# Performance work log

Hardware: AMD Instinct MI355X
Metric: run time of the kernel (lower is better)

The kernel has to match this reference:

```python
import jax, jax.numpy as jnp
import numpy as np

F_LEN = 21          # function_length
D_LEN = 41          # distribution_length
SLOPE = 1.0         # function_slope (nonzero -> tanh branch)
EPS = 1e-12         # torch F.normalize eps


def setup_inputs() -> dict:
    key = jax.random.key(0)
    k1, k2, k3, k4, k5 = jax.random.split(key, 5)
    B, L = 64, 2048
    S = F_LEN + D_LEN - 1  # 61, segment length required by the sliding slices
    lines_feature = jax.random.normal(k1, (B, L, 16), dtype=jnp.float32)
    pf = jax.random.uniform(k2, (B, L, S), dtype=jnp.float32, minval=0.1, maxval=1.0)
    pb = jax.random.uniform(k3, (B, L, S), dtype=jnp.float32, minval=0.1, maxval=1.0)
    slop = jax.random.uniform(k4, (B, L), dtype=jnp.float32, minval=0.5, maxval=2.5)
    amp = jax.random.uniform(k5, (B, L), dtype=jnp.float32, minval=0.1, maxval=0.4)
    return {
        "lines_feature": lines_feature,
        "lines_image_pf_segments": pf,
        "lines_image_pb_segments": pb,
        "lines_slop": slop,
        "lines_amplitude": amp,
    }


def reference(lines_feature, lines_image_pf_segments, lines_image_pb_segments,
              lines_slop, lines_amplitude):
    # lookup functions f/b over the function window  [B, L, F]
    x = jnp.arange(F_LEN, dtype=jnp.float32) - (F_LEN - 1) / 2.0
    lf = 0.5 - lines_amplitude[..., None] * jnp.tanh(x / (2.0 * lines_slop[..., None]))
    lb = 1.0 - lf

    # minimum variance floor (Laplace vs Gaussian)
    min_var_laplace = 1.0 / (2.0 * jnp.square(jnp.arctanh(2.0 * lines_amplitude)))
    min_var = jnp.maximum(min_var_laplace, lines_slop)

    # all D_LEN overlapping windows of length F_LEN, gathered in one shot
    idx = jnp.arange(D_LEN)[:, None] + jnp.arange(F_LEN)[None, :]   # [D, F]
    pf_win = lines_image_pf_segments[..., idx]                      # [B, L, D, F]
    pb_win = lines_image_pb_segments[..., idx]                      # [B, L, D, F]

    # log-domain product reduction over the window
    logp = jnp.log(pf_win * lf[..., None, :] + pb_win * lb[..., None, :]).sum(-1)
    dist = jnp.exp(logp)                                            # [B, L, D]

    # L1 normalize (torch.nn.functional.normalize, p=1)
    dist = dist / jnp.maximum(jnp.sum(jnp.abs(dist), axis=-1, keepdims=True), EPS)

    # line_distribution_extractor is identity pass-through of the distributions

    # Gaussian moment fit
    step = jnp.arange(D_LEN, dtype=jnp.float32)                     # [D]
    mean_tmp = jnp.sum(step * dist, axis=-1)                        # [B, L]
    var_tmp = jnp.sum(jnp.square(step - mean_tmp[..., None]) * dist, axis=-1)
    mean = mean_tmp - (D_LEN - 1) / 2.0
    var = jnp.maximum(var_tmp, min_var)
    return dist, mean, 1.0 / var
```

## Files before the change

### kernel.cpp

```cpp
#include <hip/hip_runtime.h>
#include <math.h>

#define F_LEN 21
#define D_LEN 41
#define S_LEN 61
#define ROWS 8
#define THREADS 64
#define NELEM (ROWS * S_LEN)
#define NV4   (NELEM / 4)
#define DOUT  (ROWS * D_LEN)
#define DV4   (DOUT / 4)

template <int CTRL>
__device__ __forceinline__ float dpp_add(float x) {
    int y = __builtin_amdgcn_update_dpp(0, __float_as_int(x), CTRL, 0xf, 0xf, true);
    return x + __int_as_float(y);
}
#define DPP_XOR1 0xB1
#define DPP_XOR2 0x4E
#define DPP_XOR7 0x141

__global__ __launch_bounds__(THREADS, 4) void bp_kernel(
    const float* __restrict__ pf_g, const float* __restrict__ pb_g,
    const float* __restrict__ slop_g, const float* __restrict__ amp_g,
    float* __restrict__ out_dist, float* __restrict__ out_mean,
    float* __restrict__ out_ivar)
{
    __shared__ float2 lds_fb[NELEM];

    const int tid  = threadIdx.x;
    const int rl   = tid >> 3;
    const int q    = tid & 7;
    const int row0 = blockIdx.x * ROWS;
    const int r    = row0 + rl;

    const float4* pf4 = (const float4*)(pf_g + (size_t)row0 * S_LEN);
    const float4* pb4 = (const float4*)(pb_g + (size_t)row0 * S_LEN);
    #pragma unroll
    for (int it = 0; it < 2; ++it) {
        int idx4 = it * THREADS + tid;
        if (idx4 < NV4) {
            float4 f = pf4[idx4];
            float4 b = pb4[idx4];
            lds_fb[idx4 * 4 + 0] = make_float2(f.x, b.x);
            lds_fb[idx4 * 4 + 1] = make_float2(f.y, b.y);
            lds_fb[idx4 * 4 + 2] = make_float2(f.z, b.z);
            lds_fb[idx4 * 4 + 3] = make_float2(f.w, b.w);
        }
    }

    const float a  = amp_g[r];
    const float sl = slop_g[r];

    float lf[F_LEN];
    lf[10] = 0.5f;
    {
        const float E1 = __expf(1.0f / sl);
        const float E2 = E1 * E1;
        const float E4 = E2 * E2;
        const float E8 = E4 * E4;
        float Ek[11];
        Ek[1] = E1;        Ek[2] = E2;        Ek[3] = E2 * E1;
        Ek[4] = E4;        Ek[5] = E4 * E1;   Ek[6] = E4 * E2;
        Ek[7] = E4 * Ek[3];Ek[8] = E8;        Ek[9] = E8 * E1;
        Ek[10] = E8 * E2;
        #pragma unroll
        for (int k = 1; k <= 10; ++k) {
            float rcp = __frcp_rn(Ek[k] + 1.0f);
            float dl  = a * ((Ek[k] - 1.0f) * rcp);
            lf[10 + k] = 0.5f - dl;
            lf[10 - k] = 0.5f + dl;
        }
    }

    __syncthreads();

    const int  d0   = q * 5;
    const bool has6 = (q == 7);
    const int  base = rl * S_LEN + d0;

    float prod[6] = {1.0f, 1.0f, 1.0f, 1.0f, 1.0f, 1.0f};
    #pragma unroll
    for (int i = 0; i < 26; ++i) {
        float2 fb = lds_fb[base + i];
        float  df = fb.x - fb.y;
        #pragma unroll
        for (int dp = 0; dp < 6; ++dp) {
            const int j = i - dp;
            if (j >= 0 && j < F_LEN) {
                float t = fmaf(lf[j], df, fb.y);
                if (dp == 5) t = has6 ? t : 1.0f;
                prod[dp] *= t;
            }
        }
    }

    const float df0 = (float)d0;
    float s0 = 0.0f, s1 = 0.0f, s2 = 0.0f;
    #pragma unroll
    for (int dp = 0; dp < 6; ++dp) {
        float p = prod[dp];
        if (dp == 5) p = has6 ? p : 0.0f;
        float dv = df0 + (float)dp;
        s0 += p;
        s1 += dv * p;
        s2 += dv * dv * p;
    }
    s0 = dpp_add<DPP_XOR1>(s0); s0 = dpp_add<DPP_XOR2>(s0); s0 = dpp_add<DPP_XOR7>(s0);
    s1 = dpp_add<DPP_XOR1>(s1); s1 = dpp_add<DPP_XOR2>(s1); s1 = dpp_add<DPP_XOR7>(s1);
    s2 = dpp_add<DPP_XOR1>(s2); s2 = dpp_add<DPP_XOR2>(s2); s2 = dpp_add<DPP_XOR7>(s2);

    const float inv      = 1.0f / fmaxf(s0, 1e-12f);
    const float mean_tmp = s1 * inv;
    const float m2       = s2 * inv;
    const float var_tmp  = fmaf(-mean_tmp, mean_tmp, m2);

    if (q == 0) {
        const float two_a = 2.0f * a;
        const float at    = 0.5f * __logf((1.0f + two_a) / (1.0f - two_a));
        const float min_v = fmaxf(0.5f / (at * at), sl);
        const float var   = fmaxf(var_tmp, min_v);
        out_mean[r] = mean_tmp - (float)((D_LEN - 1) / 2);
        out_ivar[r] = 1.0f / var;
    }

    __syncthreads();
    float* ldsd = (float*)lds_fb;
    #pragma unroll
    for (int dp = 0; dp < 5; ++dp)
        ldsd[rl * D_LEN + d0 + dp] = prod[dp] * inv;
    if (has6)
        ldsd[rl * D_LEN + 40] = prod[5] * inv;
    __syncthreads();

    const float4* ld4 = (const float4*)ldsd;
    float4* o4 = (float4*)(out_dist + (size_t)row0 * D_LEN);
    #pragma unroll
    for (int it = 0; it < 2; ++it) {
        int idx4 = it * THREADS + tid;
        if (idx4 < DV4) o4[idx4] = ld4[idx4];
    }
}

extern "C" void kernel_launch(void* const* d_in, const int* in_sizes, int n_in,
                              void* d_out, int out_size, void* d_ws, size_t ws_size,
                              hipStream_t stream) {
    const float* pf   = (const float*)d_in[1];
    const float* pb   = (const float*)d_in[2];
    const float* slop = (const float*)d_in[3];
    const float* amp  = (const float*)d_in[4];

    const int rows = in_sizes[3];

    float* out_dist = (float*)d_out;
    float* out_mean = out_dist + (size_t)rows * D_LEN;
    float* out_ivar = out_mean + rows;

    const int blocks = rows / ROWS;
    bp_kernel<<<blocks, THREADS, 0, stream>>>(pf, pb, slop, amp,
                                              out_dist, out_mean, out_ivar);
}
```

Before: 26.90 us.

## Process four tiles per block with double-buffered direct global-to-LDS loads

```diff
diff --git a/kernel.cpp b/kernel.cpp
--- a/kernel.cpp
+++ b/kernel.cpp
@@ -5,11 +5,12 @@
 #define D_LEN 41
 #define S_LEN 61
 #define ROWS 8
+#define TILES 4
 #define THREADS 64
-#define NELEM (ROWS * S_LEN)
-#define NV4   (NELEM / 4)
-#define DOUT  (ROWS * D_LEN)
-#define DV4   (DOUT / 4)
+#define TFLO (ROWS * S_LEN)
+#define TPAD 512
+#define DOUTT (ROWS * D_LEN)
+#define DV4T (DOUTT / 4)
 
 template <int CTRL>
 __device__ __forceinline__ float dpp_add(float x) {
@@ -20,125 +21,158 @@
 #define DPP_XOR2 0x4E
 #define DPP_XOR7 0x141
 
+__device__ __forceinline__ void gll16(const float* g, float* l) {
+    __builtin_amdgcn_global_load_lds(
+        (const __attribute__((address_space(1))) void*)g,
+        (__attribute__((address_space(3))) void*)l, 16, 0, 0);
+}
+
+__device__ __forceinline__ void stage_tile(const float* pf_g, const float* pb_g,
+                                           float* bufF, float* bufB,
+                                           int row0, int lane) {
+    const float* gf = pf_g + (size_t)row0 * S_LEN;
+    const float* gb = pb_g + (size_t)row0 * S_LEN;
+    gll16(gf + lane * 4, bufF);
+    gll16(gb + lane * 4, bufB);
+    if (lane < 58) {
+        gll16(gf + 256 + lane * 4, bufF + 256);
+        gll16(gb + 256 + lane * 4, bufB + 256);
+    }
+}
+
+#define FENCE() do { asm volatile("" ::: "memory"); \
+                     __builtin_amdgcn_sched_barrier(0); } while (0)
+
 __global__ __launch_bounds__(THREADS, 4) void bp_kernel(
     const float* __restrict__ pf_g, const float* __restrict__ pb_g,
     const float* __restrict__ slop_g, const float* __restrict__ amp_g,
     float* __restrict__ out_dist, float* __restrict__ out_mean,
     float* __restrict__ out_ivar)
 {
-    __shared__ float2 lds_fb[NELEM];
+    __shared__ float ldsF[2][TPAD];
+    __shared__ float ldsB[2][TPAD];
+    __shared__ float distL[DOUTT];
 
-    const int tid  = threadIdx.x;
-    const int rl   = tid >> 3;
-    const int q    = tid & 7;
-    const int row0 = blockIdx.x * ROWS;
-    const int r    = row0 + rl;
+    const int lane = threadIdx.x;
+    const int rl   = lane >> 3;
+    const int q    = lane & 7;
+    const int brow = blockIdx.x * (TILES * ROWS);
 
-    const float4* pf4 = (const float4*)(pf_g + (size_t)row0 * S_LEN);
-    const float4* pb4 = (const float4*)(pb_g + (size_t)row0 * S_LEN);
+    float aT[TILES], sT[TILES];
     #pragma unroll
-    for (int it = 0; it < 2; ++it) {
-        int idx4 = it * THREADS + tid;
-        if (idx4 < NV4) {
-            float4 f = pf4[idx4];
-            float4 b = pb4[idx4];
-            lds_fb[idx4 * 4 + 0] = make_float2(f.x, b.x);
-            lds_fb[idx4 * 4 + 1] = make_float2(f.y, b.y);
-            lds_fb[idx4 * 4 + 2] = make_float2(f.z, b.z);
-            lds_fb[idx4 * 4 + 3] = make_float2(f.w, b.w);
-        }
+    for (int t = 0; t < TILES; ++t) {
+        aT[t] = amp_g[brow + t * ROWS + rl];
+        sT[t] = slop_g[brow + t * ROWS + rl];
     }
-
-    const float a  = amp_g[r];
-    const float sl = slop_g[r];
-
-    float lf[F_LEN];
-    lf[10] = 0.5f;
-    {
-        const float E1 = __expf(1.0f / sl);
-        const float E2 = E1 * E1;
-        const float E4 = E2 * E2;
-        const float E8 = E4 * E4;
-        float Ek[11];
-        Ek[1] = E1;        Ek[2] = E2;        Ek[3] = E2 * E1;
-        Ek[4] = E4;        Ek[5] = E4 * E1;   Ek[6] = E4 * E2;
-        Ek[7] = E4 * Ek[3];Ek[8] = E8;        Ek[9] = E8 * E1;
-        Ek[10] = E8 * E2;
-        #pragma unroll
-        for (int k = 1; k <= 10; ++k) {
-            float rcp = __frcp_rn(Ek[k] + 1.0f);
-            float dl  = a * ((Ek[k] - 1.0f) * rcp);
-            lf[10 + k] = 0.5f - dl;
-            lf[10 - k] = 0.5f + dl;
-        }
-    }
-
-    __syncthreads();
+    FENCE();
+    stage_tile(pf_g, pb_g, ldsF[0], ldsB[0], brow, lane);
+    FENCE();
+    stage_tile(pf_g, pb_g, ldsF[1], ldsB[1], brow + ROWS, lane);
+    FENCE();
 
     const int  d0   = q * 5;
     const bool has6 = (q == 7);
     const int  base = rl * S_LEN + d0;
 
-    float prod[6] = {1.0f, 1.0f, 1.0f, 1.0f, 1.0f, 1.0f};
     #pragma unroll
-    for (int i = 0; i < 26; ++i) {
-        float2 fb = lds_fb[base + i];
-        float  df = fb.x - fb.y;
+    for (int t = 0; t < TILES; ++t) {
+        if (t < TILES - 1) asm volatile("s_waitcnt vmcnt(4)" ::: "memory");
+        else               asm volatile("s_waitcnt vmcnt(0)" ::: "memory");
+        __builtin_amdgcn_sched_barrier(0);
+
+        const int   r  = brow + t * ROWS + rl;
+        const float a  = aT[t];
+        const float sl = sT[t];
+
+        float lf[F_LEN];
+        lf[10] = 0.5f;
+        {
+            const float E1 = __expf(1.0f / sl);
+            const float E2 = E1 * E1;
+            const float E4 = E2 * E2;
+            const float E8 = E4 * E4;
+            float Ek[11];
+            Ek[1] = E1;         Ek[2] = E2;       Ek[3] = E2 * E1;
+            Ek[4] = E4;         Ek[5] = E4 * E1;  Ek[6] = E4 * E2;
+            Ek[7] = E4 * Ek[3]; Ek[8] = E8;       Ek[9] = E8 * E1;
+            Ek[10] = E8 * E2;
+            #pragma unroll
+            for (int k = 1; k <= 10; ++k) {
+                float rcp = __frcp_rn(Ek[k] + 1.0f);
+                float dl  = a * ((Ek[k] - 1.0f) * rcp);
+                lf[10 + k] = 0.5f - dl;
+                lf[10 - k] = 0.5f + dl;
+            }
+        }
+
+        const float* Fb = ldsF[t & 1];
+        const float* Bb = ldsB[t & 1];
+        float prod[6] = {1.0f, 1.0f, 1.0f, 1.0f, 1.0f, 1.0f};
+        #pragma unroll
+        for (int i = 0; i < 26; ++i) {
+            float fv = Fb[base + i];
+            float bv = Bb[base + i];
+            float df = fv - bv;
+            #pragma unroll
+            for (int dp = 0; dp < 6; ++dp) {
+                const int j = i - dp;
+                if (j >= 0 && j < F_LEN) {
+                    float tm = fmaf(lf[j], df, bv);
+                    if (dp == 5) tm = has6 ? tm : 1.0f;
+                    prod[dp] *= tm;
+                }
+            }
+        }
+
+        const float df0 = (float)d0;
+        float s0 = 0.0f, s1 = 0.0f, s2 = 0.0f;
         #pragma unroll
         for (int dp = 0; dp < 6; ++dp) {
-            const int j = i - dp;
-            if (j >= 0 && j < F_LEN) {
-                float t = fmaf(lf[j], df, fb.y);
-                if (dp == 5) t = has6 ? t : 1.0f;
-                prod[dp] *= t;
-            }
+            float p = prod[dp];
+            if (dp == 5) p = has6 ? p : 0.0f;
+            float dv = df0 + (float)dp;
+            s0 += p;
+            s1 += dv * p;
+            s2 += dv * dv * p;
         }
-    }
+        s0 = dpp_add<DPP_XOR1>(s0); s0 = dpp_add<DPP_XOR2>(s0); s0 = dpp_add<DPP_XOR7>(s0);
+        s1 = dpp_add<DPP_XOR1>(s1); s1 = dpp_add<DPP_XOR2>(s1); s1 = dpp_add<DPP_XOR7>(s1);
+        s2 = dpp_add<DPP_XOR1>(s2); s2 = dpp_add<DPP_XOR2>(s2); s2 = dpp_add<DPP_XOR7>(s2);
 
-    const float df0 = (float)d0;
-    float s0 = 0.0f, s1 = 0.0f, s2 = 0.0f;
-    #pragma unroll
-    for (int dp = 0; dp < 6; ++dp) {
-        float p = prod[dp];
-        if (dp == 5) p = has6 ? p : 0.0f;
-        float dv = df0 + (float)dp;
-        s0 += p;
-        s1 += dv * p;
-        s2 += dv * dv * p;
-    }
-    s0 = dpp_add<DPP_XOR1>(s0); s0 = dpp_add<DPP_XOR2>(s0); s0 = dpp_add<DPP_XOR7>(s0);
-    s1 = dpp_add<DPP_XOR1>(s1); s1 = dpp_add<DPP_XOR2>(s1); s1 = dpp_add<DPP_XOR7>(s1);
-    s2 = dpp_add<DPP_XOR1>(s2); s2 = dpp_add<DPP_XOR2>(s2); s2 = dpp_add<DPP_XOR7>(s2);
+        const float inv      = 1.0f / fmaxf(s0, 1e-12f);
+        const float mean_tmp = s1 * inv;
+        const float m2       = s2 * inv;
+        const float var_tmp  = fmaf(-mean_tmp, mean_tmp, m2);
 
-    const float inv      = 1.0f / fmaxf(s0, 1e-12f);
-    const float mean_tmp = s1 * inv;
-    const float m2       = s2 * inv;
-    const float var_tmp  = fmaf(-mean_tmp, mean_tmp, m2);
+        asm volatile("s_waitcnt lgkmcnt(0)" ::: "memory");
+        __builtin_amdgcn_sched_barrier(0);
+        if (t + 2 < TILES)
+            stage_tile(pf_g, pb_g, ldsF[t & 1], ldsB[t & 1],
+                       brow + (t + 2) * ROWS, lane);
+        FENCE();
 
-    if (q == 0) {
-        const float two_a = 2.0f * a;
-        const float at    = 0.5f * __logf((1.0f + two_a) / (1.0f - two_a));
-        const float min_v = fmaxf(0.5f / (at * at), sl);
-        const float var   = fmaxf(var_tmp, min_v);
-        out_mean[r] = mean_tmp - (float)((D_LEN - 1) / 2);
-        out_ivar[r] = 1.0f / var;
-    }
+        if (q == 0) {
+            const float two_a = 2.0f * a;
+            const float at    = 0.5f * __logf((1.0f + two_a) / (1.0f - two_a));
+            const float min_v = fmaxf(0.5f / (at * at), sl);
+            const float var   = fmaxf(var_tmp, min_v);
+            out_mean[r] = mean_tmp - 20.0f;
+            out_ivar[r] = 1.0f / var;
+        }
 
-    __syncthreads();
-    float* ldsd = (float*)lds_fb;
-    #pragma unroll
-    for (int dp = 0; dp < 5; ++dp)
-        ldsd[rl * D_LEN + d0 + dp] = prod[dp] * inv;
-    if (has6)
-        ldsd[rl * D_LEN + 40] = prod[5] * inv;
-    __syncthreads();
+        #pragma unroll
+        for (int dp = 0; dp < 5; ++dp)
+            distL[rl * D_LEN + d0 + dp] = prod[dp] * inv;
+        if (has6)
+            distL[rl * D_LEN + 40] = prod[5] * inv;
 
-    const float4* ld4 = (const float4*)ldsd;
-    float4* o4 = (float4*)(out_dist + (size_t)row0 * D_LEN);
-    #pragma unroll
-    for (int it = 0; it < 2; ++it) {
-        int idx4 = it * THREADS + tid;
-        if (idx4 < DV4) o4[idx4] = ld4[idx4];
+        const float4* ld4 = (const float4*)distL;
+        float4* o4 = (float4*)(out_dist + (size_t)(brow + t * ROWS) * D_LEN);
+        #pragma unroll
+        for (int it = 0; it < 2; ++it) {
+            int idx4 = it * THREADS + lane;
+            if (idx4 < DV4T) o4[idx4] = ld4[idx4];
+        }
     }
 }
 
@@ -156,7 +190,7 @@
     float* out_mean = out_dist + (size_t)rows * D_LEN;
     float* out_ivar = out_mean + rows;
 
-    const int blocks = rows / ROWS;
+    const int blocks = rows / (ROWS * TILES);
     bp_kernel<<<blocks, THREADS, 0, stream>>>(pf, pb, slop, amp,
                                               out_dist, out_mean, out_ivar);
 }
```

Measured after the change: 26.94 us. No clear change (+0.1%).

## Use two-wave blocks with per-wave LDS, waitcnt sync, and shared tanh table

Applied to the files above, without the earlier changes.

```diff
diff --git a/kernel.cpp b/kernel.cpp
--- a/kernel.cpp
+++ b/kernel.cpp
@@ -4,12 +4,13 @@
 #define F_LEN 21
 #define D_LEN 41
 #define S_LEN 61
-#define ROWS 8
-#define THREADS 64
-#define NELEM (ROWS * S_LEN)
-#define NV4   (NELEM / 4)
-#define DOUT  (ROWS * D_LEN)
-#define DV4   (DOUT / 4)
+#define ROWS_W 8
+#define WAVES 2
+#define THREADS 128
+#define NELEM_W (ROWS_W * S_LEN)
+#define NV4_W (NELEM_W / 4)
+#define DOUT_W (ROWS_W * D_LEN)
+#define DV4_W (DOUT_W / 4)
 
 template <int CTRL>
 __device__ __forceinline__ float dpp_add(float x) {
@@ -20,60 +21,70 @@
 #define DPP_XOR2 0x4E
 #define DPP_XOR7 0x141
 
-__global__ __launch_bounds__(THREADS, 4) void bp_kernel(
+#define LGKM0() do { asm volatile("s_waitcnt lgkmcnt(0)" ::: "memory"); \
+                     __builtin_amdgcn_sched_barrier(0); } while (0)
+
+__global__ __launch_bounds__(THREADS, 8) void bp_kernel(
     const float* __restrict__ pf_g, const float* __restrict__ pb_g,
     const float* __restrict__ slop_g, const float* __restrict__ amp_g,
     float* __restrict__ out_dist, float* __restrict__ out_mean,
     float* __restrict__ out_ivar)
 {
-    __shared__ float2 lds_fb[NELEM];
+    __shared__ float2 lds_fb[WAVES][NELEM_W];
+    __shared__ float  dlL[WAVES][ROWS_W * 10];
 
     const int tid  = threadIdx.x;
-    const int rl   = tid >> 3;
-    const int q    = tid & 7;
-    const int row0 = blockIdx.x * ROWS;
-    const int r    = row0 + rl;
+    const int w    = tid >> 6;
+    const int lane = tid & 63;
+    const int rl   = lane >> 3;
+    const int q    = lane & 7;
+    const int wrow0 = blockIdx.x * (WAVES * ROWS_W) + w * ROWS_W;
+    const int r    = wrow0 + rl;
 
-    const float4* pf4 = (const float4*)(pf_g + (size_t)row0 * S_LEN);
-    const float4* pb4 = (const float4*)(pb_g + (size_t)row0 * S_LEN);
+    float2* fbW = lds_fb[w];
+    float*  dlW = dlL[w];
+
+    const float4* pf4 = (const float4*)(pf_g + (size_t)wrow0 * S_LEN);
+    const float4* pb4 = (const float4*)(pb_g + (size_t)wrow0 * S_LEN);
     #pragma unroll
     for (int it = 0; it < 2; ++it) {
-        int idx4 = it * THREADS + tid;
-        if (idx4 < NV4) {
+        int idx4 = it * 64 + lane;
+        if (idx4 < NV4_W) {
             float4 f = pf4[idx4];
             float4 b = pb4[idx4];
-            lds_fb[idx4 * 4 + 0] = make_float2(f.x, b.x);
-            lds_fb[idx4 * 4 + 1] = make_float2(f.y, b.y);
-            lds_fb[idx4 * 4 + 2] = make_float2(f.z, b.z);
-            lds_fb[idx4 * 4 + 3] = make_float2(f.w, b.w);
+            fbW[idx4 * 4 + 0] = make_float2(f.x, b.x);
+            fbW[idx4 * 4 + 1] = make_float2(f.y, b.y);
+            fbW[idx4 * 4 + 2] = make_float2(f.z, b.z);
+            fbW[idx4 * 4 + 3] = make_float2(f.w, b.w);
         }
     }
 
     const float a  = amp_g[r];
     const float sl = slop_g[r];
-
-    float lf[F_LEN];
-    lf[10] = 0.5f;
     {
-        const float E1 = __expf(1.0f / sl);
-        const float E2 = E1 * E1;
-        const float E4 = E2 * E2;
-        const float E8 = E4 * E4;
-        float Ek[11];
-        Ek[1] = E1;        Ek[2] = E2;        Ek[3] = E2 * E1;
-        Ek[4] = E4;        Ek[5] = E4 * E1;   Ek[6] = E4 * E2;
-        Ek[7] = E4 * Ek[3];Ek[8] = E8;        Ek[9] = E8 * E1;
-        Ek[10] = E8 * E2;
-        #pragma unroll
-        for (int k = 1; k <= 10; ++k) {
-            float rcp = __frcp_rn(Ek[k] + 1.0f);
-            float dl  = a * ((Ek[k] - 1.0f) * rcp);
-            lf[10 + k] = 0.5f - dl;
-            lf[10 - k] = 0.5f + dl;
+        float* dlp = dlW + rl * 10;
+        const int k = q + 1;
+        float Ek = __expf((float)k / sl);
+        float t  = __fdividef(Ek - 1.0f, Ek + 1.0f);
+        dlp[q] = a * t;
+        if (q < 2) {
+            const int k2 = q + 9;
+            float Ek2 = __expf((float)k2 / sl);
+            float t2  = __fdividef(Ek2 - 1.0f, Ek2 + 1.0f);
+            dlp[8 + q] = a * t2;
         }
     }
 
-    __syncthreads();
+    LGKM0();
+
+    float dl_[10];
+    {
+        const float2* dp2 = (const float2*)(dlW + rl * 10);
+        float2 p0 = dp2[0], p1 = dp2[1], p2 = dp2[2], p3 = dp2[3], p4 = dp2[4];
+        dl_[0] = p0.x; dl_[1] = p0.y; dl_[2] = p1.x; dl_[3] = p1.y;
+        dl_[4] = p2.x; dl_[5] = p2.y; dl_[6] = p3.x; dl_[7] = p3.y;
+        dl_[8] = p4.x; dl_[9] = p4.y;
+    }
 
     const int  d0   = q * 5;
     const bool has6 = (q == 7);
@@ -82,13 +93,17 @@
     float prod[6] = {1.0f, 1.0f, 1.0f, 1.0f, 1.0f, 1.0f};
     #pragma unroll
     for (int i = 0; i < 26; ++i) {
-        float2 fb = lds_fb[base + i];
+        float2 fb = fbW[base + i];
         float  df = fb.x - fb.y;
+        float  h  = fmaf(0.5f, df, fb.y);
         #pragma unroll
         for (int dp = 0; dp < 6; ++dp) {
             const int j = i - dp;
             if (j >= 0 && j < F_LEN) {
-                float t = fmaf(lf[j], df, fb.y);
+                float t;
+                if (j == 10)      t = h;
+                else if (j < 10)  t = fmaf(dl_[9 - j],  df, h);
+                else              t = fmaf(dl_[j - 11], -df, h);
                 if (dp == 5) t = has6 ? t : 1.0f;
                 prod[dp] *= t;
             }
@@ -124,21 +139,21 @@
         out_ivar[r] = 1.0f / var;
     }
 
-    __syncthreads();
-    float* ldsd = (float*)lds_fb;
+    LGKM0();
+    float* ldsd = (float*)fbW;
     #pragma unroll
     for (int dp = 0; dp < 5; ++dp)
         ldsd[rl * D_LEN + d0 + dp] = prod[dp] * inv;
     if (has6)
         ldsd[rl * D_LEN + 40] = prod[5] * inv;
-    __syncthreads();
 
+    LGKM0();
     const float4* ld4 = (const float4*)ldsd;
-    float4* o4 = (float4*)(out_dist + (size_t)row0 * D_LEN);
+    float4* o4 = (float4*)(out_dist + (size_t)wrow0 * D_LEN);
     #pragma unroll
     for (int it = 0; it < 2; ++it) {
-        int idx4 = it * THREADS + tid;
-        if (idx4 < DV4) o4[idx4] = ld4[idx4];
+        int idx4 = it * 64 + lane;
+        if (idx4 < DV4_W) o4[idx4] = ld4[idx4];
     }
 }
 
@@ -156,7 +171,7 @@
     float* out_mean = out_dist + (size_t)rows * D_LEN;
     float* out_ivar = out_mean + rows;
 
-    const int blocks = rows / ROWS;
+    const int blocks = rows / (WAVES * ROWS_W);
     bp_kernel<<<blocks, THREADS, 0, stream>>>(pf, pb, slop, amp,
                                               out_dist, out_mean, out_ivar);
 }
```

Result: slower. 40.34 us (+49.9%).
